# Performance work log

Hardware: AMD Instinct MI355X
Metric: run time of the kernel (lower is better)

Reference implementation:

```python
import jax, jax.numpy as jnp
import numpy as np

N = 20000      # nodes
E = 320000     # edges (avg degree 16)
IN = 128       # in_size
H = 256        # layer_size
DEPTH = 2      # extra hidden layers
BN_EPS = 1e-5


def setup_inputs() -> dict:
    key = jax.random.key(0)
    ks = jax.random.split(key, 16)
    x = jax.random.normal(ks[0], (N, IN), jnp.float32)
    edge_index = jax.random.randint(ks[1], (2, E), 0, N)
    # first MLP layer: Linear(2*IN -> H) + BatchNorm1d(H) (inference stats)
    W0 = jax.random.normal(ks[2], (H, 2 * IN), jnp.float32) * 0.05
    b0 = jnp.zeros((H,), jnp.float32)
    g0 = jnp.ones((H,), jnp.float32)
    beta0 = jnp.zeros((H,), jnp.float32)
    m0 = jax.random.normal(ks[3], (H,), jnp.float32) * 0.1
    v0 = jax.random.uniform(ks[4], (H,), jnp.float32, 0.5, 1.5)
    # DEPTH repeated layers: Linear(H -> H) + BatchNorm1d(H)
    Ws = jax.random.normal(ks[5], (DEPTH, H, H), jnp.float32) * 0.05
    bs = jnp.zeros((DEPTH, H), jnp.float32)
    gs = jnp.ones((DEPTH, H), jnp.float32)
    betas = jnp.zeros((DEPTH, H), jnp.float32)
    ms = jax.random.normal(ks[6], (DEPTH, H), jnp.float32) * 0.1
    vs = jax.random.uniform(ks[7], (DEPTH, H), jnp.float32, 0.5, 1.5)
    return {"x": x, "edge_index": edge_index,
            "W0": W0, "b0": b0, "g0": g0, "beta0": beta0, "m0": m0, "v0": v0,
            "Ws": Ws, "bs": bs, "gs": gs, "betas": betas, "ms": ms, "vs": vs}


def _bn(h, g, b, m, v):
    # BatchNorm1d in inference mode (running stats)
    return (h - m) * (g * jax.lax.rsqrt(v + BN_EPS)) + b


def reference(x, edge_index, W0, b0, g0, beta0, m0, v0, Ws, bs, gs, betas, ms, vs):
    src = edge_index[0]  # x_j (source / neighbor)
    dst = edge_index[1]  # x_i (target), also scatter index
    # gather + concat: [E, 2*IN]
    h = jnp.concatenate([x[dst], x[src]], axis=-1)
    # edge MLP (dropout is identity in eval mode)
    h = jax.nn.selu(_bn(h @ W0.T + b0, g0, beta0, m0, v0))
    for i in range(DEPTH):
        h = jax.nn.selu(_bn(h @ Ws[i].T + bs[i], gs[i], betas[i], ms[i], vs[i]))
    # scatter-mean aggregation onto target nodes
    agg_sum = jax.ops.segment_sum(h, dst, num_segments=N)
    cnt = jax.ops.segment_sum(jnp.ones((E,), h.dtype), dst, num_segments=N)
    agg = agg_sum / jnp.maximum(cnt, 1.0)[:, None]
    return (agg, h)  # (aggregated node features, edge activations)
```

## Files before the change

kernel.cpp:

```cpp
#include <hip/hip_runtime.h>
#include <hip/hip_bf16.h>

#define IN_F 128
#define HF 256
#define BN_EPS 1e-5f
#define SELU_SCALE 1.0507009873554805f
#define SELU_ALPHA 1.6732632423543772f

typedef __attribute__((ext_vector_type(8))) _Float16 half8;
typedef __attribute__((ext_vector_type(2))) unsigned int u32x2;
typedef __attribute__((ext_vector_type(4))) float f32x4;

__device__ __forceinline__ short f2h(float f) {
    _Float16 h = (_Float16)f;
    return __builtin_bit_cast(short, h);
}

__device__ __forceinline__ float selu_f(float x) {
    const float SA = SELU_SCALE * SELU_ALPHA;
    float e = __expf(x);
    return x > 0.f ? SELU_SCALE * x : SA * e - SA;
}

__device__ __forceinline__ unsigned int pk2h(float a, float b) {
    return __builtin_bit_cast(unsigned int, __builtin_amdgcn_cvt_pkrtz(a, b));
}

__device__ __forceinline__ void gld_lds16(const void* g, void* l) {
    __builtin_amdgcn_global_load_lds(
        (const __attribute__((address_space(1))) unsigned int*)g,
        (__attribute__((address_space(3))) unsigned int*)l, 16, 0, 0);
}

__global__ void prep_kernel(const float* __restrict__ W0, const float* __restrict__ b0,
                            const float* __restrict__ g0, const float* __restrict__ beta0,
                            const float* __restrict__ m0, const float* __restrict__ v0,
                            const float* __restrict__ Ws, const float* __restrict__ bs,
                            const float* __restrict__ gs, const float* __restrict__ betas,
                            const float* __restrict__ ms, const float* __restrict__ vs,
                            unsigned short* __restrict__ Wf, float* __restrict__ biasArr) {
    int b = blockIdx.x;
    int layer = b >> 8;
    int n = b & 255;
    int k = threadIdx.x;
    const float *W, *bb, *g, *be, *m, *v;
    if (layer == 0) { W = W0; bb = b0; g = g0; be = beta0; m = m0; v = v0; }
    else {
        int i = layer - 1;
        W = Ws + (size_t)i * HF * HF; bb = bs + i * HF; g = gs + i * HF;
        be = betas + i * HF; m = ms + i * HF; v = vs + i * HF;
    }
    float s = g[n] * rsqrtf(v[n] + BN_EPS);
    int kk = k >> 5, kc = (k >> 3) & 3, j = k & 7;
    Wf[((((size_t)layer * 8 + kk) * 4 + kc) * 256 + n) * 8 + j] =
        (unsigned short)f2h(W[n * HF + k] * s);
    if (k == 0) biasArr[layer * HF + n] = (bb[n] - m[n]) * s + be[n];
}

__global__ void count_kernel(const int* __restrict__ dstI, int* __restrict__ cnt, int E) {
    int i = blockIdx.x * 256 + threadIdx.x;
    if (i < E) atomicAdd(cnt + dstI[i], 1);
}

__global__ void scan_local(int* __restrict__ cnt, int* __restrict__ wrk,
                           int* __restrict__ btot, int n) {
    __shared__ int s[1024];
    int b = blockIdx.x, t = threadIdx.x, i = b * 1024 + t;
    int v = (i < n) ? cnt[i] : 0;
    s[t] = v;
    __syncthreads();
#pragma unroll
    for (int d = 1; d < 1024; d <<= 1) {
        int add = (t >= d) ? s[t - d] : 0;
        __syncthreads();
        s[t] += add;
        __syncthreads();
    }
    if (i < n) {
        wrk[i] = s[t] - v;
        ((float*)cnt)[i] = 1.f / fmaxf((float)v, 1.f);
    }
    if (t == 1023) btot[b] = s[1023];
}
__global__ void scan_tops(int* __restrict__ btot, int nb) {
    if (threadIdx.x == 0) {
        int run = 0;
        for (int i = 0; i < nb; ++i) { int v = btot[i]; btot[i] = run; run += v; }
    }
}
__global__ void scan_add(int* __restrict__ wrk, const int* __restrict__ btot, int n) {
    int i = blockIdx.x * 1024 + threadIdx.x;
    if (i < n) wrk[i] += btot[blockIdx.x];
}

__global__ void scatter_kernel(const int* __restrict__ dstI, int* __restrict__ wrk,
                               int* __restrict__ perm, int E) {
    int i = blockIdx.x * 256 + threadIdx.x;
    if (i < E) {
        int p = atomicAdd(wrk + dstI[i], 1);
        perm[p] = i;
    }
}

__global__ __launch_bounds__(256, 3)
void fused_kernel(const float* __restrict__ x,
                  const int* __restrict__ dstI, const int* __restrict__ srcI,
                  const int* __restrict__ perm,
                  const unsigned char* __restrict__ Wfb,
                  const float* __restrict__ biasArr,
                  const float* __restrict__ invA,
                  unsigned char* __restrict__ hB, float* __restrict__ agg) {
    __shared__ __align__(16) unsigned char lds[49152];
    __shared__ int peL[64];
    __shared__ int pdL[64];

    const int base = blockIdx.x * 64;
    const int t = threadIdx.x;
    const int lane = t & 63;
    const int w = t >> 6;
    const int lrow = lane & 15;
    const int lgrp = lane >> 4;

    auto stageB = [&](int L, int kk) {
        const unsigned char* src = Wfb + ((size_t)(L * 8 + kk) << 14);
        unsigned char* dstBase = lds + 32768 + w * 1024;
#pragma unroll
        for (int i = 0; i < 4; ++i)
            gld_lds16(src + (i * 256 + t) * 16, dstBase + i * 4096);
    };
    auto readA = [&](int kk, int mi) -> half8 {
        int row = mi * 16 + lrow;
        return *(const half8*)&lds[row * 512 +
            ((kk * 64 + lgrp * 16) ^ ((row & 7) << 4))];
    };

    stageB(0, 0);

    {
        int r = t >> 2, q = t & 3;
        int e = perm[base + r];
        int idx = (q < 2 ? dstI : srcI)[e];
        const float* xr = x + (size_t)idx * IN_F + (q & 1) * 64;
        int swz = (r & 7) << 4;
#pragma unroll
        for (int u = 0; u < 16; ++u) {
            f32x4 v = *(const f32x4*)(xr + u * 4);
            u32x2 hv = {pk2h(v[0], v[1]), pk2h(v[2], v[3])};
            *(u32x2*)&lds[r * 512 + ((q * 128 + u * 8) ^ swz)] = hv;
        }
    }

    f32x4 acc[4][4];
    const f32x4 zero = {0.f, 0.f, 0.f, 0.f};

#pragma unroll
    for (int L = 0; L < 3; ++L) {
#pragma unroll
        for (int mi = 0; mi < 4; ++mi)
#pragma unroll
            for (int ni = 0; ni < 4; ++ni) acc[mi][ni] = zero;

        half8 af_c[4], af_n[4];
#pragma unroll
        for (int kk = 0; kk < 8; ++kk) {
            __syncthreads();

            if (kk == 0) {
#pragma unroll
                for (int mi = 0; mi < 4; ++mi) af_c[mi] = readA(0, mi);
            }
            half8 bf[4];
#pragma unroll
            for (int ni = 0; ni < 4; ++ni)
                bf[ni] = *(const half8*)&lds[32768 + lgrp * 4096 +
                                             (w * 64 + ni * 16 + lrow) * 16];
            __syncthreads();

            if (kk < 7) stageB(L, kk + 1);
            else if (L < 2) stageB(L + 1, 0);

            if (kk < 7) {
#pragma unroll
                for (int mi = 0; mi < 4; ++mi) af_n[mi] = readA(kk + 1, mi);
            }

            if (L < 2) {
#pragma unroll
                for (int mi = 0; mi < 4; ++mi)
#pragma unroll
                    for (int ni = 0; ni < 4; ++ni)
                        acc[mi][ni] = __builtin_amdgcn_mfma_f32_16x16x32_f16(
                            bf[ni], af_c[mi], acc[mi][ni], 0, 0, 0);
            } else {
#pragma unroll
                for (int mi = 0; mi < 4; ++mi)
#pragma unroll
                    for (int ni = 0; ni < 4; ++ni)
                        acc[mi][ni] = __builtin_amdgcn_mfma_f32_16x16x32_f16(
                            af_c[mi], bf[ni], acc[mi][ni], 0, 0, 0);
            }
            if (kk < 7) {
#pragma unroll
                for (int mi = 0; mi < 4; ++mi) af_c[mi] = af_n[mi];
            }
        }

        if (L < 2) {
#pragma unroll
            for (int ni = 0; ni < 4; ++ni) {
                f32x4 bv = *(const f32x4*)(biasArr + L * HF + w * 64 + ni * 16 + lgrp * 4);
#pragma unroll
                for (int mi = 0; mi < 4; ++mi) {
                    int row = mi * 16 + lrow;
                    float v0 = selu_f(acc[mi][ni][0] + bv[0]);
                    float v1 = selu_f(acc[mi][ni][1] + bv[1]);
                    float v2 = selu_f(acc[mi][ni][2] + bv[2]);
                    float v3 = selu_f(acc[mi][ni][3] + bv[3]);
                    u32x2 d = {pk2h(v0, v1), pk2h(v2, v3)};
                    *(u32x2*)&lds[row * 512 +
                        ((w * 128 + ni * 32 + lgrp * 8) ^ ((row & 7) << 4))] = d;
                }
            }
        } else {
            if (t < 64) {
                int e = perm[base + t];
                peL[t] = e;
                pdL[t] = dstI[e];
            }
            float bc[4];
#pragma unroll
            for (int ni = 0; ni < 4; ++ni) bc[ni] = biasArr[2 * HF + w * 64 + ni * 16 + lrow];
            unsigned char* EP = lds + 32768;
            int curD = -1;
            float carry = 0.f;
#pragma unroll
            for (int cc = 0; cc < 4; ++cc) {
                if (cc) __syncthreads();
#pragma unroll
                for (int ni = 0; ni < 4; ++ni)
#pragma unroll
                    for (int r = 0; r < 4; ++r) {
                        int er = lgrp * 4 + r;
                        int cg = w * 64 + ni * 16 + lrow;
                        float val = selu_f(acc[cc][ni][r] + bc[ni]);
                        *(float*)&EP[er * 1024 + ((cg * 4) ^ ((er & 7) << 4))] = val;
                    }
                __syncthreads();
#pragma unroll
                for (int i = 0; i < 4; ++i) {
                    int f = t + i * 256;
                    int row = f >> 6, ch = f & 63;
                    f32x4 v = *(const f32x4*)&EP[row * 1024 + ((ch * 16) ^ ((row & 7) << 4))];
                    *(f32x4*)(hB + (size_t)peL[cc * 16 + row] * 1024 + ch * 16) = v;
                }
#pragma unroll
                for (int r = 0; r < 16; ++r) {
                    float v = *(const float*)&EP[r * 1024 + ((t * 4) ^ ((r & 7) << 4))];
                    int d = pdL[cc * 16 + r];
                    if (d != curD) {
                        if (curD >= 0)
                            atomicAdd(agg + (size_t)curD * HF + t, carry * invA[curD]);
                        carry = 0.f;
                        curD = d;
                    }
                    carry += v;
                }
            }
            atomicAdd(agg + (size_t)curD * HF + t, carry * invA[curD]);
        }
    }
}

extern "C" void kernel_launch(void* const* d_in, const int* in_sizes, int n_in,
                              void* d_out, int out_size, void* d_ws, size_t ws_size,
                              hipStream_t stream) {
    const float* x     = (const float*)d_in[0];
    const int*   ei    = (const int*)d_in[1];
    const float* W0    = (const float*)d_in[2];
    const float* b0    = (const float*)d_in[3];
    const float* g0    = (const float*)d_in[4];
    const float* beta0 = (const float*)d_in[5];
    const float* m0    = (const float*)d_in[6];
    const float* v0    = (const float*)d_in[7];
    const float* Ws    = (const float*)d_in[8];
    const float* bs    = (const float*)d_in[9];
    const float* gs    = (const float*)d_in[10];
    const float* betas = (const float*)d_in[11];
    const float* ms    = (const float*)d_in[12];
    const float* vs    = (const float*)d_in[13];

    const int Nn = in_sizes[0] / IN_F;
    const int E  = in_sizes[1] / 2;

    float* agg  = (float*)d_out;
    float* hptr = agg + (size_t)Nn * HF;

    char* wsb = (char*)d_ws;
    unsigned short* Wf = (unsigned short*)wsb;
    float* biasArr = (float*)(wsb + 393216);
    int* cnt  = (int*)(wsb + 396288);
    int* wrk  = (int*)(wsb + 476288);
    int* perm = (int*)(wsb + 556288);
    int* btot = (int*)agg;

    const int* srcI = ei;
    const int* dstI = ei + E;

    const int nScan = (Nn + 1023) / 1024;

    prep_kernel<<<3 * HF, HF, 0, stream>>>(W0, b0, g0, beta0, m0, v0,
                                           Ws, bs, gs, betas, ms, vs, Wf, biasArr);
    hipMemsetAsync(cnt, 0, (size_t)Nn * sizeof(int), stream);
    count_kernel<<<(E + 255) / 256, 256, 0, stream>>>(dstI, cnt, E);
    scan_local<<<nScan, 1024, 0, stream>>>(cnt, wrk, btot, Nn);
    scan_tops<<<1, 64, 0, stream>>>(btot, nScan);
    scan_add<<<nScan, 1024, 0, stream>>>(wrk, btot, Nn);
    hipMemsetAsync(agg, 0, (size_t)Nn * HF * sizeof(float), stream);
    scatter_kernel<<<(E + 255) / 256, 256, 0, stream>>>(dstI, wrk, perm, E);

    fused_kernel<<<E / 64, 256, 0, stream>>>(x, dstI, srcI, perm,
                                             (const unsigned char*)Wf, biasArr,
                                             (const float*)cnt,
                                             (unsigned char*)hptr, agg);
}
```

Before: 271.7 us.

## Double-buffer weight tiles in LDS with vmcnt-based waits and MFMA priority

Weight k-slices go into two LDS buffers, prefetched two stages ahead. Each stage waits on vmcnt for its own buffer and uses raw s_barrier instead of full __syncthreads. This is meant to overlap global-to-LDS weight loads with MFMA work and cut barrier stalls, and s_setprio raises wave priority around the MFMA block. In exchange LDS grows to 64KB and launch bounds drop to 2 blocks per CU, lowering occupancy. The peL/pdL arrays move into the reused LDS region.

```diff
diff --git a/kernel.cpp b/kernel.cpp
--- a/kernel.cpp
+++ b/kernel.cpp
@@ -102,7 +102,7 @@
     }
 }
 
-__global__ __launch_bounds__(256, 3)
+__global__ __launch_bounds__(256, 2)
 void fused_kernel(const float* __restrict__ x,
                   const int* __restrict__ dstI, const int* __restrict__ srcI,
                   const int* __restrict__ perm,
@@ -110,9 +110,7 @@
                   const float* __restrict__ biasArr,
                   const float* __restrict__ invA,
                   unsigned char* __restrict__ hB, float* __restrict__ agg) {
-    __shared__ __align__(16) unsigned char lds[49152];
-    __shared__ int peL[64];
-    __shared__ int pdL[64];
+    __shared__ __align__(16) unsigned char lds[65536];
 
     const int base = blockIdx.x * 64;
     const int t = threadIdx.x;
@@ -121,9 +119,9 @@
     const int lrow = lane & 15;
     const int lgrp = lane >> 4;
 
-    auto stageB = [&](int L, int kk) {
-        const unsigned char* src = Wfb + ((size_t)(L * 8 + kk) << 14);
-        unsigned char* dstBase = lds + 32768 + w * 1024;
+    auto stageB = [&](int s) {
+        const unsigned char* src = Wfb + ((size_t)s << 14);
+        unsigned char* dstBase = lds + 32768 + (s & 1) * 16384 + w * 1024;
 #pragma unroll
         for (int i = 0; i < 4; ++i)
             gld_lds16(src + (i * 256 + t) * 16, dstBase + i * 4096);
@@ -134,7 +132,7 @@
             ((kk * 64 + lgrp * 16) ^ ((row & 7) << 4))];
     };
 
-    stageB(0, 0);
+    stageB(0);
 
     {
         int r = t >> 2, q = t & 3;
@@ -149,6 +147,9 @@
             *(u32x2*)&lds[r * 512 + ((q * 128 + u * 8) ^ swz)] = hv;
         }
     }
+    stageB(1);
+    asm volatile("s_waitcnt lgkmcnt(0)" ::: "memory");
+    __builtin_amdgcn_sched_barrier(0);
 
     f32x4 acc[4][4];
     const f32x4 zero = {0.f, 0.f, 0.f, 0.f};
@@ -163,7 +164,13 @@
         half8 af_c[4], af_n[4];
 #pragma unroll
         for (int kk = 0; kk < 8; ++kk) {
-            __syncthreads();
+            const int s = L * 8 + kk;
+            const int p = s & 1;
+
+            if (s < 23) asm volatile("s_waitcnt vmcnt(4)" ::: "memory");
+            else        asm volatile("s_waitcnt vmcnt(0)" ::: "memory");
+            __builtin_amdgcn_s_barrier();
+            __builtin_amdgcn_sched_barrier(0);
 
             if (kk == 0) {
 #pragma unroll
@@ -172,18 +179,21 @@
             half8 bf[4];
 #pragma unroll
             for (int ni = 0; ni < 4; ++ni)
-                bf[ni] = *(const half8*)&lds[32768 + lgrp * 4096 +
+                bf[ni] = *(const half8*)&lds[32768 + p * 16384 + lgrp * 4096 +
                                              (w * 64 + ni * 16 + lrow) * 16];
-            __syncthreads();
-
-            if (kk < 7) stageB(L, kk + 1);
-            else if (L < 2) stageB(L + 1, 0);
+            asm volatile("s_waitcnt lgkmcnt(0)" ::: "memory");
+            __builtin_amdgcn_sched_barrier(0);
+            __builtin_amdgcn_s_barrier();
+            __builtin_amdgcn_sched_barrier(0);
+
+            if (s + 2 < 24) stageB(s + 2);
 
             if (kk < 7) {
 #pragma unroll
                 for (int mi = 0; mi < 4; ++mi) af_n[mi] = readA(kk + 1, mi);
             }
 
+            __builtin_amdgcn_s_setprio(1);
             if (L < 2) {
 #pragma unroll
                 for (int mi = 0; mi < 4; ++mi)
@@ -199,6 +209,7 @@
                         acc[mi][ni] = __builtin_amdgcn_mfma_f32_16x16x32_f16(
                             af_c[mi], bf[ni], acc[mi][ni], 0, 0, 0);
             }
+            __builtin_amdgcn_s_setprio(0);
             if (kk < 7) {
 #pragma unroll
                 for (int mi = 0; mi < 4; ++mi) af_c[mi] = af_n[mi];
@@ -221,12 +232,16 @@
                         ((w * 128 + ni * 32 + lgrp * 8) ^ ((row & 7) << 4))] = d;
                 }
             }
+            asm volatile("s_waitcnt lgkmcnt(0)" ::: "memory");
+            __builtin_amdgcn_sched_barrier(0);
         } else {
             if (t < 64) {
                 int e = perm[base + t];
-                peL[t] = e;
-                pdL[t] = dstI[e];
-            }
+                ((int*)lds)[t] = e;
+                ((int*)lds)[64 + t] = dstI[e];
+            }
+            const int* peL = (const int*)lds;
+            const int* pdL = (const int*)lds + 64;
             float bc[4];
 #pragma unroll
             for (int ni = 0; ni < 4; ++ni) bc[ni] = biasArr[2 * HF + w * 64 + ni * 16 + lrow];
```

Result: slower. 296.2 us (+9.0%).
